# Kernel optimization log

Hardware: AMD Instinct MI355X
Metric: run time of the kernel (lower is better)

The kernel has to match this reference:

```python
import jax, jax.numpy as jnp
import numpy as np

B, N, D = 4096, 16384, 1024

def setup_inputs() -> dict:
    key = jax.random.key(0)
    k1, k2, k3 = jax.random.split(key, 3)
    x = jax.random.normal(k1, (B, D), dtype=jnp.float32)
    cache_image_features = jax.random.normal(k2, (N, D), dtype=jnp.float32)
    cache_text_features = jax.random.normal(k3, (N, D), dtype=jnp.float32)
    beta = jnp.ones((1,), dtype=jnp.float32)
    alpha = jnp.ones((1,), dtype=jnp.float32)
    return {
        "x": x,
        "cache_image_features": cache_image_features,
        "cache_text_features": cache_text_features,
        "beta": beta,
        "alpha": alpha,
    }

def reference(x, cache_image_features, cache_text_features, beta, alpha):
    # similarity: [B, N] = x @ keys^T
    similarity = jnp.einsum("bd,nd->bn", x, cache_image_features)
    # softmax over cache entries, scaled by beta
    weights = jax.nn.softmax(beta * similarity, axis=-1)
    # retrieve text features: [B, D]
    retrieved = jnp.einsum("bn,nd->bd", weights, cache_text_features)
    return x + alpha * retrieved
```

## Files before the change

### kernel.cpp

```cpp
#include <hip/hip_runtime.h>


typedef float    f32x4  __attribute__((ext_vector_type(4)));
typedef _Float16 f16x8  __attribute__((ext_vector_type(8)));
typedef _Float16 f16x4  __attribute__((ext_vector_type(4)));

#define LOG2E 1.44269504088896340736f
#define MAXSEL 1024
#define KK 1024
#define NT 16

__device__ __forceinline__ void lds_load16(const void* g, void* l) {
    __builtin_amdgcn_global_load_lds(
        (__attribute__((address_space(1))) void*)(uintptr_t)g,
        (__attribute__((address_space(3))) void*)l,
        16, 0, 0);
}

template<int N> __device__ __forceinline__ void vwait() {
    if constexpr (N == 8)      asm volatile("s_waitcnt vmcnt(8)" ::: "memory");
    else if constexpr (N == 6) asm volatile("s_waitcnt vmcnt(6)" ::: "memory");
    else if constexpr (N == 4) asm volatile("s_waitcnt vmcnt(4)" ::: "memory");
    else if constexpr (N == 0) asm volatile("s_waitcnt vmcnt(0)" ::: "memory");
}

__global__ void convert_f32_f16(const float* __restrict__ a, _Float16* __restrict__ o, long n4) {
    long i = (long)blockIdx.x * blockDim.x + threadIdx.x;
    if (i < n4) {
        f32x4 f = ((const f32x4*)a)[i];
        ((f16x4*)o)[i] = __builtin_convertvector(f, f16x4);
    }
}

__device__ __forceinline__ void stage_half(const _Float16* __restrict__ g,
                                           int k0, _Float16* lds_half, int tid) {
    const int r = tid >> 3;
    const int c = ((tid & 7) - (r & 7)) & 7;
    const _Float16* s0 = g + (long)r * KK + k0 + c * 8;
    _Float16* d = lds_half + (tid >> 6) * 512;
    lds_load16(s0, d);
    lds_load16(s0 + 64 * KK, d + 4096);
}

template<bool IA1, bool IB1, bool IA0, bool IB0, int D2, int D1>
__device__ __forceinline__ void tile_body(
    _Float16* Ac, _Float16* Bc, _Float16* An, _Float16* Bn,
    const _Float16* __restrict__ Ag, const _Float16* __restrict__ Bg, int kt,
    const int (&aoff)[4][2], const int (&boff)[2][2],
    int tid, f32x4 (&acc)[2][4][2][2])
{
    f16x8 a[4][2];
    f16x8 b[2][2][2];

#pragma unroll
    for (int mi = 0; mi < 4; ++mi)
#pragma unroll
        for (int ks = 0; ks < 2; ++ks)
            a[mi][ks] = *(const f16x8*)&Ac[aoff[mi][ks]];
#pragma unroll
    for (int nj = 0; nj < 2; ++nj)
#pragma unroll
        for (int ks = 0; ks < 2; ++ks)
            b[0][nj][ks] = *(const f16x8*)&Bc[boff[nj][ks]];
    if (IA1) stage_half(Ag + 128L * KK, (kt + 1) * 64, An + 8192, tid);
    __builtin_amdgcn_s_barrier();
    asm volatile("s_waitcnt lgkmcnt(0)" ::: "memory");
    __builtin_amdgcn_sched_barrier(0);
    __builtin_amdgcn_s_setprio(1);
#pragma unroll
    for (int mi = 0; mi < 4; ++mi)
#pragma unroll
        for (int nj = 0; nj < 2; ++nj)
#pragma unroll
            for (int ks = 0; ks < 2; ++ks)
                acc[0][mi][0][nj] = __builtin_amdgcn_mfma_f32_16x16x32_f16(
                    a[mi][ks], b[0][nj][ks], acc[0][mi][0][nj], 0, 0, 0);
    __builtin_amdgcn_s_setprio(0);
    vwait<D2>();
    __builtin_amdgcn_s_barrier();

#pragma unroll
    for (int nj = 0; nj < 2; ++nj)
#pragma unroll
        for (int ks = 0; ks < 2; ++ks)
            b[1][nj][ks] = *(const f16x8*)&Bc[boff[nj][ks] + 8192];
    if (IB1) stage_half(Bg + 128L * KK, (kt + 1) * 64, Bn + 8192, tid);
    __builtin_amdgcn_s_barrier();
    asm volatile("s_waitcnt lgkmcnt(0)" ::: "memory");
    __builtin_amdgcn_sched_barrier(0);
    __builtin_amdgcn_s_setprio(1);
#pragma unroll
    for (int mi = 0; mi < 4; ++mi)
#pragma unroll
        for (int nj = 0; nj < 2; ++nj)
#pragma unroll
            for (int ks = 0; ks < 2; ++ks)
                acc[0][mi][1][nj] = __builtin_amdgcn_mfma_f32_16x16x32_f16(
                    a[mi][ks], b[1][nj][ks], acc[0][mi][1][nj], 0, 0, 0);
    __builtin_amdgcn_s_setprio(0);
    __builtin_amdgcn_s_barrier();

#pragma unroll
    for (int mi = 0; mi < 4; ++mi)
#pragma unroll
        for (int ks = 0; ks < 2; ++ks)
            a[mi][ks] = *(const f16x8*)&Ac[aoff[mi][ks] + 8192];
    if (IA0) stage_half(Ag, (kt + 2) * 64, Ac, tid);
    __builtin_amdgcn_s_barrier();
    asm volatile("s_waitcnt lgkmcnt(0)" ::: "memory");
    __builtin_amdgcn_sched_barrier(0);
    __builtin_amdgcn_s_setprio(1);
#pragma unroll
    for (int mi = 0; mi < 4; ++mi)
#pragma unroll
        for (int nj = 0; nj < 2; ++nj)
#pragma unroll
            for (int ks = 0; ks < 2; ++ks)
                acc[1][mi][0][nj] = __builtin_amdgcn_mfma_f32_16x16x32_f16(
                    a[mi][ks], b[0][nj][ks], acc[1][mi][0][nj], 0, 0, 0);
    __builtin_amdgcn_s_setprio(0);
    __builtin_amdgcn_s_barrier();

    if (IB0) stage_half(Bg, (kt + 2) * 64, Bc, tid);
    __builtin_amdgcn_s_barrier();
    __builtin_amdgcn_s_setprio(1);
#pragma unroll
    for (int mi = 0; mi < 4; ++mi)
#pragma unroll
        for (int nj = 0; nj < 2; ++nj)
#pragma unroll
            for (int ks = 0; ks < 2; ++ks)
                acc[1][mi][1][nj] = __builtin_amdgcn_mfma_f32_16x16x32_f16(
                    a[mi][ks], b[1][nj][ks], acc[1][mi][1][nj], 0, 0, 0);
    __builtin_amdgcn_s_setprio(0);
    vwait<D1>();
    __builtin_amdgcn_s_barrier();
}

__global__ __launch_bounds__(512, 2) void gemm_bt_f16_256(
    const _Float16* __restrict__ A,
    const _Float16* __restrict__ Bm,
    _Float16* __restrict__ C,
    int Mtiles, int N)
{
    __shared__ _Float16 sm[65536];
    const int tid  = threadIdx.x;
    const int lane = tid & 63;
    const int wave = tid >> 6;
    const int wm = wave >> 2;
    const int wn = wave & 3;

    const int nwg = (int)gridDim.x;
    const int bid = (int)blockIdx.x;
    const int swz = (bid & 7) * (nwg >> 3) + (bid >> 3);
    const int bm = swz % Mtiles;
    const int bn = swz / Mtiles;

    const _Float16* Ag = A  + (long)bm * 256 * KK;
    const _Float16* Bg = Bm + (long)bn * 256 * KK;

    const int r15 = lane & 15;
    const int kq  = lane >> 4;
    int aoff[4][2], boff[2][2];
#pragma unroll
    for (int mi = 0; mi < 4; ++mi)
#pragma unroll
        for (int ks = 0; ks < 2; ++ks) {
            int R = wm * 64 + mi * 16 + r15;
            int c = ks * 4 + kq;
            aoff[mi][ks] = R * 64 + (((c + (R & 7)) & 7) * 8);
        }
#pragma unroll
    for (int nj = 0; nj < 2; ++nj)
#pragma unroll
        for (int ks = 0; ks < 2; ++ks) {
            int R = wn * 32 + nj * 16 + r15;
            int c = ks * 4 + kq;
            boff[nj][ks] = R * 64 + (((c + (R & 7)) & 7) * 8);
        }

    _Float16* A0b = sm;
    _Float16* B0b = sm + 16384;
    _Float16* A1b = sm + 32768;
    _Float16* B1b = sm + 49152;

    f32x4 acc[2][4][2][2] = {};

    stage_half(Ag,           0,  A0b,        tid);
    stage_half(Bg,           0,  B0b,        tid);
    stage_half(Ag + 128L*KK, 0,  A0b + 8192, tid);
    stage_half(Bg + 128L*KK, 0,  B0b + 8192, tid);
    stage_half(Ag,           64, A1b,        tid);
    stage_half(Bg,           64, B1b,        tid);
    vwait<8>();
    __builtin_amdgcn_s_barrier();

    for (int t = 0; t < NT - 2; t += 2) {
        tile_body<true,true,true,true,6,8>(A0b,B0b, A1b,B1b, Ag,Bg, t,   aoff,boff,tid,acc);
        tile_body<true,true,true,true,6,8>(A1b,B1b, A0b,B0b, Ag,Bg, t+1, aoff,boff,tid,acc);
    }
    tile_body<true,true,false,false,6,4>(A0b,B0b, A1b,B1b, Ag,Bg, NT-2, aoff,boff,tid,acc);
    tile_body<false,false,false,false,0,-1>(A1b,B1b, A0b,B0b, Ag,Bg, NT-1, aoff,boff,tid,acc);

    const long rb0 = (long)bm * 256 + wm * 64 + (lane >> 4) * 4;
    const long cb0 = (long)bn * 256 + wn * 32 + (lane & 15);
#pragma unroll
    for (int mh = 0; mh < 2; ++mh)
#pragma unroll
    for (int mi = 0; mi < 4; ++mi)
#pragma unroll
    for (int nh = 0; nh < 2; ++nh)
#pragma unroll
    for (int nj = 0; nj < 2; ++nj) {
        const long r0 = rb0 + mh * 128 + mi * 16;
        const long c0 = cb0 + nh * 128 + nj * 16;
#pragma unroll
        for (int reg = 0; reg < 4; ++reg)
            C[(r0 + reg) * (long)N + c0] = (_Float16)acc[mh][mi][nh][nj][reg];
    }
}

__global__ __launch_bounds__(256) void softmax_gather(
    const _Float16* __restrict__ S,
    const float* __restrict__ V,
    const float* __restrict__ X,
    float* __restrict__ Out,
    const float* __restrict__ beta_p,
    const float* __restrict__ alpha_p,
    int N, int D)
{
    const int row  = blockIdx.x;
    const int tid  = threadIdx.x;
    const int lane = tid & 63;
    const int wave = tid >> 6;
    const float beta  = beta_p[0];
    const float alpha = alpha_p[0];

    __shared__ float redm[4];
    __shared__ float redl[4];
    __shared__ int   cnt;
    __shared__ int   sel_idx[MAXSEL];
    __shared__ float sel_w[MAXSEL];

    const f16x8* s8 = (const f16x8*)(S + (size_t)row * N);

    f32x4 v[16];
    float m = -3.4e38f;
#pragma unroll
    for (int j = 0; j < 8; ++j) {
        f16x8 h = s8[tid + j * 256];
        f32x4 lo, hiv;
#pragma unroll
        for (int c = 0; c < 4; ++c) { lo[c] = (float)h[c] * beta; hiv[c] = (float)h[c + 4] * beta; }
        v[2 * j] = lo; v[2 * j + 1] = hiv;
        m = fmaxf(m, fmaxf(fmaxf(lo[0], lo[1]), fmaxf(lo[2], lo[3])));
        m = fmaxf(m, fmaxf(fmaxf(hiv[0], hiv[1]), fmaxf(hiv[2], hiv[3])));
    }
#pragma unroll
    for (int off = 32; off; off >>= 1) m = fmaxf(m, __shfl_xor(m, off));
    if (lane == 0) redm[wave] = m;
    if (tid == 0) cnt = 0;
    __syncthreads();
    m = fmaxf(fmaxf(redm[0], redm[1]), fmaxf(redm[2], redm[3]));

    float l = 0.f;
#pragma unroll
    for (int j = 0; j < 16; ++j) {
        f32x4 e;
#pragma unroll
        for (int c = 0; c < 4; ++c) e[c] = exp2f((v[j][c] - m) * LOG2E);
        l += e[0] + e[1] + e[2] + e[3];
        v[j] = e;
    }
#pragma unroll
    for (int off = 32; off; off >>= 1) l += __shfl_xor(l, off);
    if (lane == 0) redl[wave] = l;
    __syncthreads();
    l = redl[0] + redl[1] + redl[2] + redl[3];

#pragma unroll
    for (int j = 0; j < 16; ++j) {
#pragma unroll
        for (int c = 0; c < 4; ++c) {
            float e = v[j][c];
            if (e >= 3.0e-7f) {
                int p = atomicAdd(&cnt, 1);
                if (p < MAXSEL) {
                    sel_idx[p] = (tid + (j >> 1) * 256) * 8 + (j & 1) * 4 + c;
                    sel_w[p]   = e;
                }
            }
        }
    }
    __syncthreads();
    int nsel = cnt; if (nsel > MAXSEL) nsel = MAXSEL;

    const float wscale = alpha / l;
    f32x4 acc = {0.f, 0.f, 0.f, 0.f};
    for (int i = 0; i < nsel; ++i) {
        const float w = sel_w[i] * wscale;
        const f32x4 t = *(const f32x4*)(V + (size_t)sel_idx[i] * D + tid * 4);
        acc += w * t;
    }
    const f32x4 xr = ((const f32x4*)(X + (size_t)row * D))[tid];
    ((f32x4*)(Out + (size_t)row * D))[tid] = xr + acc;
}

extern "C" void kernel_launch(void* const* d_in, const int* in_sizes, int n_in,
                              void* d_out, int out_size, void* d_ws, size_t ws_size,
                              hipStream_t stream) {
    const float* x     = (const float*)d_in[0];
    const float* kimg  = (const float*)d_in[1];
    const float* vtxt  = (const float*)d_in[2];
    const float* beta  = (const float*)d_in[3];
    const float* alpha = (const float*)d_in[4];
    float* out = (float*)d_out;

    const int D = 1024;
    const int B = in_sizes[0] / D;
    const int N = in_sizes[1] / D;

    char* ws = (char*)d_ws;
    _Float16* x16 = (_Float16*)ws;
    _Float16* k16 = (_Float16*)(ws + (size_t)B * D * 2);
    _Float16* S   = (_Float16*)(ws + (size_t)B * D * 2 + (size_t)N * D * 2);

    const size_t fixed = (size_t)B * D * 2 + (size_t)N * D * 2;
    size_t avail = ws_size > fixed ? ws_size - fixed : 0;
    long Rl = (long)(avail / ((size_t)N * 2));
    Rl &= ~255L;
    int R = (int)(Rl > B ? B : Rl);
    if (R < 256) R = 256;

    {
        long nx4 = (long)B * D / 4;
        long nk4 = (long)N * D / 4;
        convert_f32_f16<<<(unsigned)((nk4 + 255) / 256), 256, 0, stream>>>(kimg, k16, nk4);
        convert_f32_f16<<<(unsigned)((nx4 + 255) / 256), 256, 0, stream>>>(x, x16, nx4);
    }

    for (int r0 = 0; r0 < B; r0 += R) {
        int Rc = B - r0; if (Rc > R) Rc = R;
        int Mtiles = Rc / 256;
        dim3 g1((unsigned)(Mtiles * (N / 256)));
        gemm_bt_f16_256<<<g1, 512, 0, stream>>>(x16 + (size_t)r0 * D, k16, S, Mtiles, N);
        softmax_gather<<<(unsigned)Rc, 256, 0, stream>>>(
            S, vtxt, x + (size_t)r0 * D, out + (size_t)r0 * D, beta, alpha, N, D);
    }
}
```

Before: 325.8 us.

## Prefetch MFMA fragments across tiles, fuse converts, add nontemporal and softmax skips

Result: slower. 454.0 us (+39.3%).

```diff
diff --git a/kernel.cpp b/kernel.cpp
--- a/kernel.cpp
+++ b/kernel.cpp
@@ -24,11 +24,18 @@
     else if constexpr (N == 0) asm volatile("s_waitcnt vmcnt(0)" ::: "memory");
 }
 
-__global__ void convert_f32_f16(const float* __restrict__ a, _Float16* __restrict__ o, long n4) {
+__device__ __forceinline__ float fexp2(float x) {
+    float r; asm("v_exp_f32 %0, %1" : "=v"(r) : "v"(x)); return r;
+}
+
+__global__ void convert2(const float* __restrict__ a, _Float16* __restrict__ oa, long na4,
+                         const float* __restrict__ b, _Float16* __restrict__ ob, long nb4) {
     long i = (long)blockIdx.x * blockDim.x + threadIdx.x;
-    if (i < n4) {
-        f32x4 f = ((const f32x4*)a)[i];
-        ((f16x4*)o)[i] = __builtin_convertvector(f, f16x4);
+    if (i < na4) {
+        ((f16x4*)oa)[i] = __builtin_convertvector(((const f32x4*)a)[i], f16x4);
+    } else {
+        long j = i - na4;
+        if (j < nb4) ((f16x4*)ob)[j] = __builtin_convertvector(((const f32x4*)b)[j], f16x4);
     }
 }
 
@@ -42,26 +49,14 @@
     lds_load16(s0 + 64 * KK, d + 4096);
 }
 
-template<bool IA1, bool IB1, bool IA0, bool IB0, int D2, int D1>
+template<bool IA1, bool IB1, bool IA0, bool IB0, bool RN, int D2, int D1>
 __device__ __forceinline__ void tile_body(
     _Float16* Ac, _Float16* Bc, _Float16* An, _Float16* Bn,
     const _Float16* __restrict__ Ag, const _Float16* __restrict__ Bg, int kt,
     const int (&aoff)[4][2], const int (&boff)[2][2],
-    int tid, f32x4 (&acc)[2][4][2][2])
+    int tid, f32x4 (&acc)[2][4][2][2],
+    f16x8 (&al)[4][2], f16x8 (&ah)[4][2], f16x8 (&bl)[2][2], f16x8 (&bh)[2][2])
 {
-    f16x8 a[4][2];
-    f16x8 b[2][2][2];
-
-#pragma unroll
-    for (int mi = 0; mi < 4; ++mi)
-#pragma unroll
-        for (int ks = 0; ks < 2; ++ks)
-            a[mi][ks] = *(const f16x8*)&Ac[aoff[mi][ks]];
-#pragma unroll
-    for (int nj = 0; nj < 2; ++nj)
-#pragma unroll
-        for (int ks = 0; ks < 2; ++ks)
-            b[0][nj][ks] = *(const f16x8*)&Bc[boff[nj][ks]];
     if (IA1) stage_half(Ag + 128L * KK, (kt + 1) * 64, An + 8192, tid);
     __builtin_amdgcn_s_barrier();
     asm volatile("s_waitcnt lgkmcnt(0)" ::: "memory");
@@ -74,17 +69,38 @@
 #pragma unroll
             for (int ks = 0; ks < 2; ++ks)
                 acc[0][mi][0][nj] = __builtin_amdgcn_mfma_f32_16x16x32_f16(
-                    a[mi][ks], b[0][nj][ks], acc[0][mi][0][nj], 0, 0, 0);
+                    al[mi][ks], bl[nj][ks], acc[0][mi][0][nj], 0, 0, 0);
     __builtin_amdgcn_s_setprio(0);
     vwait<D2>();
-    __builtin_amdgcn_s_barrier();
-
 #pragma unroll
     for (int nj = 0; nj < 2; ++nj)
 #pragma unroll
         for (int ks = 0; ks < 2; ++ks)
-            b[1][nj][ks] = *(const f16x8*)&Bc[boff[nj][ks] + 8192];
+            bh[nj][ks] = *(const f16x8*)&Bc[boff[nj][ks] + 8192];
+    __builtin_amdgcn_s_barrier();
+
+#pragma unroll
+    for (int mi = 0; mi < 4; ++mi)
+#pragma unroll
+        for (int ks = 0; ks < 2; ++ks)
+            ah[mi][ks] = *(const f16x8*)&Ac[aoff[mi][ks] + 8192];
     if (IB1) stage_half(Bg + 128L * KK, (kt + 1) * 64, Bn + 8192, tid);
+    __builtin_amdgcn_s_barrier();
+    asm volatile("s_waitcnt lgkmcnt(8)" ::: "memory");
+    __builtin_amdgcn_sched_barrier(0);
+    __builtin_amdgcn_s_setprio(1);
+#pragma unroll
+    for (int mi = 0; mi < 4; ++mi)
+#pragma unroll
+        for (int nj = 0; nj < 2; ++nj)
+#pragma unroll
+            for (int ks = 0; ks < 2; ++ks)
+                acc[0][mi][1][nj] = __builtin_amdgcn_mfma_f32_16x16x32_f16(
+                    al[mi][ks], bh[nj][ks], acc[0][mi][1][nj], 0, 0, 0);
+    __builtin_amdgcn_s_setprio(0);
+    __builtin_amdgcn_s_barrier();
+
+    if (IA0) stage_half(Ag, (kt + 2) * 64, Ac, tid);
     __builtin_amdgcn_s_barrier();
     asm volatile("s_waitcnt lgkmcnt(0)" ::: "memory");
     __builtin_amdgcn_sched_barrier(0);
@@ -95,20 +111,13 @@
         for (int nj = 0; nj < 2; ++nj)
 #pragma unroll
             for (int ks = 0; ks < 2; ++ks)
-                acc[0][mi][1][nj] = __builtin_amdgcn_mfma_f32_16x16x32_f16(
-                    a[mi][ks], b[1][nj][ks], acc[0][mi][1][nj], 0, 0, 0);
+                acc[1][mi][0][nj] = __builtin_amdgcn_mfma_f32_16x16x32_f16(
+                    ah[mi][ks], bl[nj][ks], acc[1][mi][0][nj], 0, 0, 0);
     __builtin_amdgcn_s_setprio(0);
     __builtin_amdgcn_s_barrier();
 
-#pragma unroll
-    for (int mi = 0; mi < 4; ++mi)
-#pragma unroll
-        for (int ks = 0; ks < 2; ++ks)
-            a[mi][ks] = *(const f16x8*)&Ac[aoff[mi][ks] + 8192];
-    if (IA0) stage_half(Ag, (kt + 2) * 64, Ac, tid);
-    __builtin_amdgcn_s_barrier();
-    asm volatile("s_waitcnt lgkmcnt(0)" ::: "memory");
-    __builtin_amdgcn_sched_barrier(0);
+    if (IB0) stage_half(Bg, (kt + 2) * 64, Bc, tid);
+    __builtin_amdgcn_s_barrier();
     __builtin_amdgcn_s_setprio(1);
 #pragma unroll
     for (int mi = 0; mi < 4; ++mi)
@@ -116,24 +125,22 @@
         for (int nj = 0; nj < 2; ++nj)
 #pragma unroll
             for (int ks = 0; ks < 2; ++ks)
-                acc[1][mi][0][nj] = __builtin_amdgcn_mfma_f32_16x16x32_f16(
-                    a[mi][ks], b[0][nj][ks], acc[1][mi][0][nj], 0, 0, 0);
-    __builtin_amdgcn_s_setprio(0);
-    __builtin_amdgcn_s_barrier();
-
-    if (IB0) stage_half(Bg, (kt + 2) * 64, Bc, tid);
-    __builtin_amdgcn_s_barrier();
-    __builtin_amdgcn_s_setprio(1);
-#pragma unroll
-    for (int mi = 0; mi < 4; ++mi)
-#pragma unroll
-        for (int nj = 0; nj < 2; ++nj)
-#pragma unroll
-            for (int ks = 0; ks < 2; ++ks)
                 acc[1][mi][1][nj] = __builtin_amdgcn_mfma_f32_16x16x32_f16(
-                    a[mi][ks], b[1][nj][ks], acc[1][mi][1][nj], 0, 0, 0);
+                    ah[mi][ks], bh[nj][ks], acc[1][mi][1][nj], 0, 0, 0);
     __builtin_amdgcn_s_setprio(0);
     vwait<D1>();
+    if (RN) {
+#pragma unroll
+        for (int mi = 0; mi < 4; ++mi)
+#pragma unroll
+            for (int ks = 0; ks < 2; ++ks)
+                al[mi][ks] = *(const f16x8*)&An[aoff[mi][ks]];
+#pragma unroll
+        for (int nj = 0; nj < 2; ++nj)
+#pragma unroll
+            for (int ks = 0; ks < 2; ++ks)
+                bl[nj][ks] = *(const f16x8*)&Bn[boff[nj][ks]];
+    }
     __builtin_amdgcn_s_barrier();
 }
 
@@ -185,6 +192,7 @@
     _Float16* B1b = sm + 49152;
 
     f32x4 acc[2][4][2][2] = {};
+    f16x8 al[4][2], ah[4][2], bl[2][2], bh[2][2];
 
     stage_half(Ag,           0,  A0b,        tid);
     stage_half(Bg,           0,  B0b,        tid);
@@ -194,13 +202,23 @@
     stage_half(Bg,           64, B1b,        tid);
     vwait<8>();
     __builtin_amdgcn_s_barrier();
+#pragma unroll
+    for (int mi = 0; mi < 4; ++mi)
+#pragma unroll
+        for (int ks = 0; ks < 2; ++ks)
+            al[mi][ks] = *(const f16x8*)&A0b[aoff[mi][ks]];
+#pragma unroll
+    for (int nj = 0; nj < 2; ++nj)
+#pragma unroll
+        for (int ks = 0; ks < 2; ++ks)
+            bl[nj][ks] = *(const f16x8*)&B0b[boff[nj][ks]];
 
     for (int t = 0; t < NT - 2; t += 2) {
-        tile_body<true,true,true,true,6,8>(A0b,B0b, A1b,B1b, Ag,Bg, t,   aoff,boff,tid,acc);
-        tile_body<true,true,true,true,6,8>(A1b,B1b, A0b,B0b, Ag,Bg, t+1, aoff,boff,tid,acc);
-    }
-    tile_body<true,true,false,false,6,4>(A0b,B0b, A1b,B1b, Ag,Bg, NT-2, aoff,boff,tid,acc);
-    tile_body<false,false,false,false,0,-1>(A1b,B1b, A0b,B0b, Ag,Bg, NT-1, aoff,boff,tid,acc);
+        tile_body<true,true,true,true,true,6,8>(A0b,B0b, A1b,B1b, Ag,Bg, t,   aoff,boff,tid,acc, al,ah,bl,bh);
+        tile_body<true,true,true,true,true,6,8>(A1b,B1b, A0b,B0b, Ag,Bg, t+1, aoff,boff,tid,acc, al,ah,bl,bh);
+    }
+    tile_body<true,true,false,false,true,6,4>(A0b,B0b, A1b,B1b, Ag,Bg, NT-2, aoff,boff,tid,acc, al,ah,bl,bh);
+    tile_body<false,false,false,false,false,0,-1>(A1b,B1b, A0b,B0b, Ag,Bg, NT-1, aoff,boff,tid,acc, al,ah,bl,bh);
 
     const long rb0 = (long)bm * 256 + wm * 64 + (lane >> 4) * 4;
     const long cb0 = (long)bn * 256 + wn * 32 + (lane & 15);
@@ -216,11 +234,12 @@
         const long c0 = cb0 + nh * 128 + nj * 16;
 #pragma unroll
         for (int reg = 0; reg < 4; ++reg)
-            C[(r0 + reg) * (long)N + c0] = (_Float16)acc[mh][mi][nh][nj][reg];
-    }
-}
-
-__global__ __launch_bounds__(256) void softmax_gather(
+            __builtin_nontemporal_store((_Float16)acc[mh][mi][nh][nj][reg],
+                                        &C[(r0 + reg) * (long)N + c0]);
+    }
+}
+
+__global__ __launch_bounds__(256, 4) void softmax_gather(
     const _Float16* __restrict__ S,
     const float* __restrict__ V,
     const float* __restrict__ X,
@@ -248,7 +267,7 @@
     float m = -3.4e38f;
 #pragma unroll
     for (int j = 0; j < 8; ++j) {
-        f16x8 h = s8[tid + j * 256];
+        f16x8 h = __builtin_nontemporal_load(s8 + tid + j * 256);
         f32x4 lo, hiv;
 #pragma unroll
         for (int c = 0; c < 4; ++c) { lo[c] = (float)h[c] * beta; hiv[c] = (float)h[c + 4] * beta; }
@@ -256,6 +275,7 @@
         m = fmaxf(m, fmaxf(fmaxf(lo[0], lo[1]), fmaxf(lo[2], lo[3])));
         m = fmaxf(m, fmaxf(fmaxf(hiv[0], hiv[1]), fmaxf(hiv[2], hiv[3])));
     }
+    const float lm = m;
 #pragma unroll
     for (int off = 32; off; off >>= 1) m = fmaxf(m, __shfl_xor(m, off));
     if (lane == 0) redm[wave] = m;
@@ -263,14 +283,17 @@
     __syncthreads();
     m = fmaxf(fmaxf(redm[0], redm[1]), fmaxf(redm[2], redm[3]));
 
+    const bool active = (lm >= m - 15.f);
     float l = 0.f;
-#pragma unroll
-    for (int j = 0; j < 16; ++j) {
-        f32x4 e;
-#pragma unroll
-        for (int c = 0; c < 4; ++c) e[c] = exp2f((v[j][c] - m) * LOG2E);
-        l += e[0] + e[1] + e[2] + e[3];
-        v[j] = e;
+    if (active) {
+#pragma unroll
+        for (int j = 0; j < 16; ++j) {
+            f32x4 e;
+#pragma unroll
+            for (int c = 0; c < 4; ++c) e[c] = fexp2((v[j][c] - m) * LOG2E);
+            l += e[0] + e[1] + e[2] + e[3];
+            v[j] = e;
+        }
     }
 #pragma unroll
     for (int off = 32; off; off >>= 1) l += __shfl_xor(l, off);
@@ -278,16 +301,18 @@
     __syncthreads();
     l = redl[0] + redl[1] + redl[2] + redl[3];
 
-#pragma unroll
-    for (int j = 0; j < 16; ++j) {
-#pragma unroll
-        for (int c = 0; c < 4; ++c) {
-            float e = v[j][c];
-            if (e >= 3.0e-7f) {
-                int p = atomicAdd(&cnt, 1);
-                if (p < MAXSEL) {
-                    sel_idx[p] = (tid + (j >> 1) * 256) * 8 + (j & 1) * 4 + c;
-                    sel_w[p]   = e;
+    if (active) {
+#pragma unroll
+        for (int j = 0; j < 16; ++j) {
+#pragma unroll
+            for (int c = 0; c < 4; ++c) {
+                float e = v[j][c];
+                if (e >= 3.0e-7f) {
+                    int p = atomicAdd(&cnt, 1);
+                    if (p < MAXSEL) {
+                        sel_idx[p] = (tid + (j >> 1) * 256) * 8 + (j & 1) * 4 + c;
+                        sel_w[p]   = e;
+                    }
                 }
             }
         }
@@ -303,7 +328,8 @@
         acc += w * t;
     }
     const f32x4 xr = ((const f32x4*)(X + (size_t)row * D))[tid];
-    ((f32x4*)(Out + (size_t)row * D))[tid] = xr + acc;
+    f32x4 o = xr + acc;
+    __builtin_nontemporal_store(o, (f32x4*)(Out + (size_t)row * D) + tid);
 }
 
 extern "C" void kernel_launch(void* const* d_in, const int* in_sizes, int n_in,
@@ -335,8 +361,8 @@
     {
         long nx4 = (long)B * D / 4;
         long nk4 = (long)N * D / 4;
-        convert_f32_f16<<<(unsigned)((nk4 + 255) / 256), 256, 0, stream>>>(kimg, k16, nk4);
-        convert_f32_f16<<<(unsigned)((nx4 + 255) / 256), 256, 0, stream>>>(x, x16, nx4);
+        long tot = nk4 + nx4;
+        convert2<<<(unsigned)((tot + 255) / 256), 256, 0, stream>>>(kimg, k16, nk4, x, x16, nx4);
     }
 
     for (int r0 = 0; r0 < B; r0 += R) {
```
